# Performance work log

Hardware: AMD Instinct MI355X
Metric: run time of the kernel (lower is better)

## Reference

```python
import jax, jax.numpy as jnp
import numpy as np

NUM_EXPERTS = 8


def _ffn(x, w1, b1, w2, b2):
    # x: [T, H]; w1: [8H, H]; w2: [H, 4H]
    gu = x @ w1.T + b1                      # [T, 8H]
    gate, up = jnp.split(gu, 2, axis=-1)    # each [T, 4H]
    h = jax.nn.gelu(gate, approximate=True) * up
    return h @ w2.T + b2                    # [T, H]


def setup_inputs() -> dict:
    key = jax.random.key(0)
    ks = jax.random.split(key, 4)
    H, E, F = 1024, NUM_EXPERTS, 4096
    scale = 0.02
    return {
        "x": jax.random.normal(ks[0], (4, 1024, H), dtype=jnp.float32),
        "gate_w": jax.random.normal(ks[1], (E, H), dtype=jnp.float32) * scale,
        "gate_b": jnp.zeros((E,), dtype=jnp.float32),
        "w1": jax.random.normal(ks[2], (E, 2 * F, H), dtype=jnp.float32) * scale,
        "b1": jnp.zeros((E, 2 * F), dtype=jnp.float32),
        "w2": jax.random.normal(ks[3], (E, H, F), dtype=jnp.float32) * scale,
        "b2": jnp.zeros((E, H), dtype=jnp.float32),
    }


def reference(x, gate_w, gate_b, w1, b1, w2, b2):
    B, S, H = x.shape
    E = gate_w.shape[0]
    T = B * S
    xf = x.reshape(T, H)

    logits = xf @ gate_w.T + gate_b          # [T, E]
    probs = jax.nn.softmax(logits, axis=-1)
    vals, idx = jax.lax.top_k(probs, 2)      # [T, 2]

    # load balancing loss (matches torch bincount of top-1 expert)
    top1_onehot = jax.nn.one_hot(idx[:, 0], E, dtype=jnp.float32)
    frequencies = top1_onehot.sum(0) / T
    probability = probs.mean(0)
    load_balancing_loss = (probability * frequencies).mean() * float(E * E)

    # normalize top-2 scores
    total = vals.sum(axis=-1, keepdims=True)
    norm_scores = vals / total               # [T, 2]

    # per-token per-expert combine weights [T, E]
    weights = (jax.nn.one_hot(idx[:, 0], E, dtype=xf.dtype) * norm_scores[:, 0:1]
               + jax.nn.one_hot(idx[:, 1], E, dtype=xf.dtype) * norm_scores[:, 1:2])

    out = jnp.zeros_like(xf)
    for e in range(E):  # fixed small loop over experts
        out = out + weights[:, e:e + 1] * _ffn(xf, w1[e], b1[e], w2[e], b2[e])

    return out.reshape(B, S, H), load_balancing_loss
```

## Files before the change

kernel.cpp:

```cpp
#include <hip/hip_runtime.h>

#define T_TOK 4096
#define HDIM 1024
#define FDIM 4096
#define NEXP 8
#define ROWCAP 9216
#define NTILES_MAX 72

typedef __attribute__((ext_vector_type(8))) short short8;
typedef __attribute__((ext_vector_type(4))) float f32x4;

__device__ __forceinline__ unsigned short f2bf(float f) {
    unsigned int u = __builtin_bit_cast(unsigned int, f);
    u += 0x7fffu + ((u >> 16) & 1u);
    return (unsigned short)(u >> 16);
}

__device__ __forceinline__ float gelu_tanh(float x) {
    float z = 1.5957691216057308f * (x + 0.044715f * x * x * x);
    return x / (1.0f + __expf(-z));
}

__device__ __forceinline__ void gload16(const unsigned short* g, unsigned short* l) {
    __builtin_amdgcn_global_load_lds(
        (const __attribute__((address_space(1))) unsigned int*)g,
        (__attribute__((address_space(3))) unsigned int*)l, 16, 0, 0);
}

__global__ __launch_bounds__(256) void routing_kernel(
    const float* __restrict__ x, const float* __restrict__ gate_w,
    const float* __restrict__ gate_b,
    int* __restrict__ tokTop1, int* __restrict__ tokE,
    float* __restrict__ tokW, float* __restrict__ tokProbs)
{
    __shared__ float gws[NEXP * HDIM];
    int tid = threadIdx.x;
    for (int i = tid; i < NEXP * HDIM / 4; i += 256)
        ((float4*)gws)[i] = ((const float4*)gate_w)[i];
    __syncthreads();
    int lane = tid & 63;
    int t = blockIdx.x * 4 + (tid >> 6);
    float acc[NEXP];
    #pragma unroll
    for (int e = 0; e < NEXP; e++) acc[e] = 0.f;
    const float* xr = x + (size_t)t * HDIM;
    for (int k = lane; k < HDIM; k += 64) {
        float xv = xr[k];
        #pragma unroll
        for (int e = 0; e < NEXP; e++) acc[e] += xv * gws[e * HDIM + k];
    }
    #pragma unroll
    for (int e = 0; e < NEXP; e++) {
        #pragma unroll
        for (int off = 32; off >= 1; off >>= 1)
            acc[e] += __shfl_xor(acc[e], off);
    }
    if (lane == 0) {
        float m = -1e30f;
        #pragma unroll
        for (int e = 0; e < NEXP; e++) { acc[e] += gate_b[e]; m = fmaxf(m, acc[e]); }
        float p[NEXP]; float s = 0.f;
        #pragma unroll
        for (int e = 0; e < NEXP; e++) { p[e] = __expf(acc[e] - m); s += p[e]; }
        float inv = 1.f / s;
        int i0 = -1; float v0 = -1.f;
        #pragma unroll
        for (int e = 0; e < NEXP; e++) {
            p[e] *= inv;
            tokProbs[t * NEXP + e] = p[e];
            if (p[e] > v0) { v0 = p[e]; i0 = e; }
        }
        int i1 = -1; float v1 = -1.f;
        #pragma unroll
        for (int e = 0; e < NEXP; e++)
            if (e != i0 && p[e] > v1) { v1 = p[e]; i1 = e; }
        float tot = v0 + v1;
        tokTop1[t] = i0;
        tokE[2 * t] = i0; tokE[2 * t + 1] = i1;
        tokW[2 * t] = v0 / tot; tokW[2 * t + 1] = v1 / tot;
    }
}

__global__ __launch_bounds__(256) void stats_kernel(
    const int* __restrict__ tokTop1, const int* __restrict__ tokE,
    const float* __restrict__ tokProbs,
    int* __restrict__ counts, int* __restrict__ cnt1, float* __restrict__ probSum)
{
    int e = blockIdx.x, tid = threadIdx.x;
    float ps = 0.f; int c1 = 0, c = 0;
    for (int t = tid; t < T_TOK; t += 256) {
        ps += tokProbs[t * NEXP + e];
        c1 += (tokTop1[t] == e);
        c  += (tokE[2 * t] == e) + (tokE[2 * t + 1] == e);
    }
    __shared__ float sps[256]; __shared__ int sc1[256]; __shared__ int sc[256];
    sps[tid] = ps; sc1[tid] = c1; sc[tid] = c; __syncthreads();
    for (int s = 128; s > 0; s >>= 1) {
        if (tid < s) { sps[tid] += sps[tid + s]; sc1[tid] += sc1[tid + s]; sc[tid] += sc[tid + s]; }
        __syncthreads();
    }
    if (tid == 0) { probSum[e] = sps[0]; cnt1[e] = sc1[0]; counts[e] = sc[0]; }
}

__global__ void scan_loss_kernel(
    const int* __restrict__ counts, const int* __restrict__ cnt1,
    const float* __restrict__ probSum,
    int* __restrict__ offsets, int* __restrict__ cursor,
    int* __restrict__ tileE, int* __restrict__ nTiles,
    float* __restrict__ loss_out)
{
    int off = 0, nt = 0; float loss = 0.f;
    for (int e = 0; e < NEXP; e++) {
        offsets[e] = off;
        int pt = (counts[e] + 127) >> 7;
        for (int i = 0; i < pt; i++) tileE[nt++] = e;
        off += pt * 128;
        cursor[e] = 0;
        loss += probSum[e] * (float)cnt1[e];
    }
    nTiles[0] = nt;
    nTiles[1] = off;
    *loss_out = loss * 8.0f / ((float)T_TOK * (float)T_TOK);
}

__global__ __launch_bounds__(256) void assign_kernel(
    const int* __restrict__ tokE, const float* __restrict__ tokW,
    const int* __restrict__ offsets, int* __restrict__ cursor,
    int* __restrict__ rowTok, float* __restrict__ rowW)
{
    int t = blockIdx.x * 256 + threadIdx.x;
    #pragma unroll
    for (int s = 0; s < 2; s++) {
        int e = tokE[2 * t + s];
        int pos = atomicAdd(&cursor[e], 1);
        int row = offsets[e] + pos;
        rowTok[row] = t;
        rowW[row] = tokW[2 * t + s];
    }
}

__global__ __launch_bounds__(256) void convertw_kernel(
    const float* __restrict__ src, unsigned short* __restrict__ dst, long n8)
{
    long stride = (long)gridDim.x * 256;
    for (long i = (long)blockIdx.x * 256 + threadIdx.x; i < n8; i += stride) {
        const float4* s = (const float4*)src + 2 * i;
        float4 f0 = s[0], f1 = s[1];
        uint4 pk;
        pk.x = (unsigned)f2bf(f0.x) | ((unsigned)f2bf(f0.y) << 16);
        pk.y = (unsigned)f2bf(f0.z) | ((unsigned)f2bf(f0.w) << 16);
        pk.z = (unsigned)f2bf(f1.x) | ((unsigned)f2bf(f1.y) << 16);
        pk.w = (unsigned)f2bf(f1.z) | ((unsigned)f2bf(f1.w) << 16);
        ((uint4*)dst)[i] = pk;
    }
}

__global__ __launch_bounds__(256) void gather_kernel(
    const float* __restrict__ x, const int* __restrict__ rowTok,
    const int* __restrict__ offsets, const int* __restrict__ counts,
    const int* __restrict__ tileE, const int* __restrict__ nTiles,
    int chunkBase, unsigned short* __restrict__ Xc)
{
    int gr = chunkBase + blockIdx.x;
    if (gr >= nTiles[1]) return;
    int tid = threadIdx.x;
    int e = tileE[gr >> 7];
    ushort4* dst = (ushort4*)(Xc + (size_t)(gr - chunkBase) * HDIM);
    if (gr - offsets[e] < counts[e]) {
        int t = rowTok[gr];
        float4 v = ((const float4*)(x + (size_t)t * HDIM))[tid];
        ushort4 b;
        b.x = f2bf(v.x); b.y = f2bf(v.y); b.z = f2bf(v.z); b.w = f2bf(v.w);
        dst[tid] = b;
    } else {
        ushort4 z; z.x = 0; z.y = 0; z.z = 0; z.w = 0;
        dst[tid] = z;
    }
}

__global__ __launch_bounds__(256) void bias_out_kernel(
    const float* __restrict__ b2, const int* __restrict__ tokE,
    const float* __restrict__ tokW, float* __restrict__ out)
{
    int t = blockIdx.x, tid = threadIdx.x;
    int e0 = tokE[2 * t], e1 = tokE[2 * t + 1];
    float w0 = tokW[2 * t], w1 = tokW[2 * t + 1];
    float4 a = ((const float4*)(b2 + (size_t)e0 * HDIM))[tid];
    float4 b = ((const float4*)(b2 + (size_t)e1 * HDIM))[tid];
    float4 r;
    r.x = w0 * a.x + w1 * b.x; r.y = w0 * a.y + w1 * b.y;
    r.z = w0 * a.z + w1 * b.z; r.w = w0 * a.w + w1 * b.w;
    ((float4*)(out + (size_t)t * HDIM))[tid] = r;
}

template<bool WB>
__global__ __launch_bounds__(256) void gemm1_kernel(
    const unsigned short* __restrict__ Xc, const void* __restrict__ w1,
    const float* __restrict__ b1, const int* __restrict__ tileE,
    const int* __restrict__ nTiles, int chunkBase,
    unsigned short* __restrict__ hc)
{
    int gt = (chunkBase >> 7) + blockIdx.y;
    if (gt >= nTiles[0]) return;
    int e = tileE[gt];
    int localBase = gt * 128 - chunkBase;
    int cTile = blockIdx.x;

    __shared__ unsigned short As[128 * 64];
    __shared__ unsigned short Bs[128 * 64];

    int tid = threadIdx.x;
    int lane = tid & 63, wave = tid >> 6;
    int wm = wave & 1, wn = wave >> 1;
    int q = lane >> 4, c15 = lane & 15;

    const unsigned short* w1e_h = nullptr;
    const float* w1e_f = nullptr;
    if constexpr (WB) w1e_h = (const unsigned short*)w1 + (size_t)e * (2 * FDIM) * HDIM;
    else              w1e_f = (const float*)w1 + (size_t)e * (2 * FDIM) * HDIM;

    f32x4 accG[4][2], accU[4][2];
    #pragma unroll
    for (int a = 0; a < 4; a++)
        #pragma unroll
        for (int b = 0; b < 2; b++)
            #pragma unroll
            for (int c = 0; c < 4; c++) { accG[a][b][c] = 0.f; accU[a][b][c] = 0.f; }

    for (int k0 = 0; k0 < HDIM; k0 += 64) {
        __syncthreads();
        if constexpr (WB) {
            #pragma unroll
            for (int ci = 0; ci < 4; ci++) {
                int G = ci * 256 + wave * 64 + lane;
                int row = G >> 3;
                int gs = (lane & 7) ^ (row & 7);
                gload16(Xc + (size_t)(localBase + row) * HDIM + k0 + gs * 8,
                        As + (ci * 256 + wave * 64) * 8);
            }
            #pragma unroll
            for (int ci = 0; ci < 4; ci++) {
                int G = ci * 256 + wave * 64 + lane;
                int j = G >> 3;
                int gs = (lane & 7) ^ (j & 7);
                int w1row = (j < 64) ? (cTile * 64 + j) : (FDIM + cTile * 64 + (j - 64));
                gload16(w1e_h + (size_t)w1row * HDIM + k0 + gs * 8,
                        Bs + (ci * 256 + wave * 64) * 8);
            }
        } else {
            #pragma unroll
            for (int ci = 0; ci < 4; ci++) {
                int chunk = tid + 256 * ci;
                int i = chunk >> 3, kc = chunk & 7;
                uint4 av = *(const uint4*)(Xc + (size_t)(localBase + i) * HDIM + k0 + kc * 8);
                *(uint4*)(As + i * 64 + ((kc ^ (i & 7)) * 8)) = av;
            }
            #pragma unroll
            for (int ci = 0; ci < 4; ci++) {
                int chunk = tid + 256 * ci;
                int j = chunk >> 3, kc = chunk & 7;
                int w1row = (j < 64) ? (cTile * 64 + j) : (FDIM + cTile * 64 + (j - 64));
                const float* src = w1e_f + (size_t)w1row * HDIM + k0 + kc * 8;
                float4 f0 = *(const float4*)src;
                float4 f1 = *(const float4*)(src + 4);
                uint4 pk;
                pk.x = (unsigned)f2bf(f0.x) | ((unsigned)f2bf(f0.y) << 16);
                pk.y = (unsigned)f2bf(f0.z) | ((unsigned)f2bf(f0.w) << 16);
                pk.z = (unsigned)f2bf(f1.x) | ((unsigned)f2bf(f1.y) << 16);
                pk.w = (unsigned)f2bf(f1.z) | ((unsigned)f2bf(f1.w) << 16);
                *(uint4*)(Bs + j * 64 + ((kc ^ (j & 7)) * 8)) = pk;
            }
        }
        __syncthreads();
        #pragma unroll
        for (int kk = 0; kk < 64; kk += 32) {
            int slot = (((q + (kk >> 3)) ^ (c15 & 7)) & 7) * 8;
            short8 aF[4], bG[2], bU[2];
            #pragma unroll
            for (int mi = 0; mi < 4; mi++)
                aF[mi] = *(const short8*)(As + (wm * 64 + mi * 16 + c15) * 64 + slot);
            #pragma unroll
            for (int ni = 0; ni < 2; ni++) {
                bG[ni] = *(const short8*)(Bs + (wn * 32 + ni * 16 + c15) * 64 + slot);
                bU[ni] = *(const short8*)(Bs + (64 + wn * 32 + ni * 16 + c15) * 64 + slot);
            }
            #pragma unroll
            for (int mi = 0; mi < 4; mi++)
                #pragma unroll
                for (int ni = 0; ni < 2; ni++) {
                    accG[mi][ni] = __builtin_amdgcn_mfma_f32_16x16x32_bf16(aF[mi], bG[ni], accG[mi][ni], 0, 0, 0);
                    accU[mi][ni] = __builtin_amdgcn_mfma_f32_16x16x32_bf16(aF[mi], bU[ni], accU[mi][ni], 0, 0, 0);
                }
        }
    }
    const float* b1e = b1 + (size_t)e * (2 * FDIM);
    #pragma unroll
    for (int mi = 0; mi < 4; mi++)
        #pragma unroll
        for (int ni = 0; ni < 2; ni++) {
            int hcol = cTile * 64 + wn * 32 + ni * 16 + c15;
            float bg = b1e[hcol], bu = b1e[FDIM + hcol];
            #pragma unroll
            for (int r = 0; r < 4; r++) {
                int row = wm * 64 + mi * 16 + q * 4 + r;
                float g = accG[mi][ni][r] + bg;
                float u = accU[mi][ni][r] + bu;
                hc[(size_t)(localBase + row) * FDIM + hcol] = f2bf(gelu_tanh(g) * u);
            }
        }
}

template<bool WB>
__global__ __launch_bounds__(256) void gemm2_kernel(
    const unsigned short* __restrict__ hc, const void* __restrict__ w2,
    const int* __restrict__ offsets, const int* __restrict__ counts,
    const int* __restrict__ rowTok, const float* __restrict__ rowW,
    const int* __restrict__ tileE, const int* __restrict__ nTiles,
    int chunkBase, float* __restrict__ out)
{
    int gt = (chunkBase >> 7) + blockIdx.y;
    if (gt >= nTiles[0]) return;
    int e = tileE[gt];
    int localBase = gt * 128 - chunkBase;
    int rowBaseG = gt * 128;
    int cTile = blockIdx.x;

    __shared__ unsigned short As[128 * 64];
    __shared__ unsigned short Bs[128 * 64];

    int tid = threadIdx.x;
    int lane = tid & 63, wave = tid >> 6;
    int wm = wave & 1, wn = wave >> 1;
    int q = lane >> 4, c15 = lane & 15;

    const unsigned short* w2e_h = nullptr;
    const float* w2e_f = nullptr;
    if constexpr (WB) w2e_h = (const unsigned short*)w2 + (size_t)e * HDIM * FDIM;
    else              w2e_f = (const float*)w2 + (size_t)e * HDIM * FDIM;

    f32x4 acc[4][4];
    #pragma unroll
    for (int a = 0; a < 4; a++)
        #pragma unroll
        for (int b = 0; b < 4; b++)
            #pragma unroll
            for (int c = 0; c < 4; c++) acc[a][b][c] = 0.f;

    for (int k0 = 0; k0 < FDIM; k0 += 64) {
        __syncthreads();
        if constexpr (WB) {
            #pragma unroll
            for (int ci = 0; ci < 4; ci++) {
                int G = ci * 256 + wave * 64 + lane;
                int row = G >> 3;
                int gs = (lane & 7) ^ (row & 7);
                gload16(hc + (size_t)(localBase + row) * FDIM + k0 + gs * 8,
                        As + (ci * 256 + wave * 64) * 8);
            }
            #pragma unroll
            for (int ci = 0; ci < 4; ci++) {
                int G = ci * 256 + wave * 64 + lane;
                int j = G >> 3;
                int gs = (lane & 7) ^ (j & 7);
                gload16(w2e_h + (size_t)(cTile * 128 + j) * FDIM + k0 + gs * 8,
                        Bs + (ci * 256 + wave * 64) * 8);
            }
        } else {
            #pragma unroll
            for (int ci = 0; ci < 4; ci++) {
                int chunk = tid + 256 * ci;
                int i = chunk >> 3, kc = chunk & 7;
                uint4 av = *(const uint4*)(hc + (size_t)(localBase + i) * FDIM + k0 + kc * 8);
                *(uint4*)(As + i * 64 + ((kc ^ (i & 7)) * 8)) = av;
            }
            #pragma unroll
            for (int ci = 0; ci < 4; ci++) {
                int chunk = tid + 256 * ci;
                int j = chunk >> 3, kc = chunk & 7;
                const float* src = w2e_f + (size_t)(cTile * 128 + j) * FDIM + k0 + kc * 8;
                float4 f0 = *(const float4*)src;
                float4 f1 = *(const float4*)(src + 4);
                uint4 pk;
                pk.x = (unsigned)f2bf(f0.x) | ((unsigned)f2bf(f0.y) << 16);
                pk.y = (unsigned)f2bf(f0.z) | ((unsigned)f2bf(f0.w) << 16);
                pk.z = (unsigned)f2bf(f1.x) | ((unsigned)f2bf(f1.y) << 16);
                pk.w = (unsigned)f2bf(f1.z) | ((unsigned)f2bf(f1.w) << 16);
                *(uint4*)(Bs + j * 64 + ((kc ^ (j & 7)) * 8)) = pk;
            }
        }
        __syncthreads();
        #pragma unroll
        for (int kk = 0; kk < 64; kk += 32) {
            int slot = (((q + (kk >> 3)) ^ (c15 & 7)) & 7) * 8;
            short8 aF[4], bF[4];
            #pragma unroll
            for (int mi = 0; mi < 4; mi++)
                aF[mi] = *(const short8*)(As + (wm * 64 + mi * 16 + c15) * 64 + slot);
            #pragma unroll
            for (int ni = 0; ni < 4; ni++)
                bF[ni] = *(const short8*)(Bs + (wn * 64 + ni * 16 + c15) * 64 + slot);
            #pragma unroll
            for (int mi = 0; mi < 4; mi++)
                #pragma unroll
                for (int ni = 0; ni < 4; ni++)
                    acc[mi][ni] = __builtin_amdgcn_mfma_f32_16x16x32_bf16(aF[mi], bF[ni], acc[mi][ni], 0, 0, 0);
        }
    }
    #pragma unroll
    for (int mi = 0; mi < 4; mi++) {
        #pragma unroll
        for (int r = 0; r < 4; r++) {
            int row = wm * 64 + mi * 16 + q * 4 + r;
            int grow = rowBaseG + row;
            if (grow - offsets[e] < counts[e]) {
                int t = rowTok[grow];
                float w = rowW[grow];
                float* od = out + (size_t)t * HDIM + cTile * 128 + wn * 64 + c15;
                #pragma unroll
                for (int ni = 0; ni < 4; ni++)
                    atomicAdd(od + ni * 16, w * acc[mi][ni][r]);
            }
        }
    }
}

extern "C" void kernel_launch(void* const* d_in, const int* in_sizes, int n_in,
                              void* d_out, int out_size, void* d_ws, size_t ws_size,
                              hipStream_t stream) {
    (void)in_sizes; (void)n_in; (void)out_size;
    const float* x      = (const float*)d_in[0];
    const float* gate_w = (const float*)d_in[1];
    const float* gate_b = (const float*)d_in[2];
    const float* w1     = (const float*)d_in[3];
    const float* b1     = (const float*)d_in[4];
    const float* w2     = (const float*)d_in[5];
    const float* b2     = (const float*)d_in[6];
    float* out = (float*)d_out;

    char* ws = (char*)d_ws;
    int*   counts   = (int*)(ws + 0);
    int*   cnt1     = (int*)(ws + 32);
    int*   cursor   = (int*)(ws + 64);
    int*   offsets  = (int*)(ws + 96);
    float* probSum  = (float*)(ws + 128);
    int*   nTiles   = (int*)(ws + 160);
    int*   tileE    = (int*)(ws + 256);
    int*   tokTop1  = (int*)(ws + 1024);
    int*   tokE     = (int*)(ws + 1024 + 16384);
    float* tokW     = (float*)(ws + 1024 + 49152);
    float* tokProbs = (float*)(ws + 1024 + 81920);
    int*   rowTok   = (int*)(ws + 1024 + 212992);
    float* rowW     = (float*)(ws + 1024 + 249856);
    const size_t fixedEnd = 512 * 1024;

    const size_t W1E = (size_t)NEXP * 2 * FDIM * HDIM;
    const size_t W2E = (size_t)NEXP * HDIM * FDIM;
    const size_t WBYTES = (W1E + W2E) * 2;
    bool wbf16 = ws_size >= fixedEnd + WBYTES + (size_t)128 * (HDIM + FDIM) * 2;

    unsigned short* w1b = nullptr;
    unsigned short* w2b = nullptr;
    size_t chunkStart = fixedEnd;
    if (wbf16) {
        w1b = (unsigned short*)(ws + fixedEnd);
        w2b = w1b + W1E;
        chunkStart = fixedEnd + WBYTES;
    }

    size_t avail = ws_size > chunkStart ? ws_size - chunkStart : 0;
    int ch = (int)((avail / (10240ULL * 128ULL)) * 128ULL);
    if (ch > ROWCAP) ch = ROWCAP;
    if (ch < 128) ch = 128;
    unsigned short* Xc = (unsigned short*)(ws + chunkStart);
    unsigned short* hc = (unsigned short*)(ws + chunkStart + (size_t)ch * HDIM * 2);
    int nChunks = (ROWCAP + ch - 1) / ch;

    if (wbf16) {
        convertw_kernel<<<2048, 256, 0, stream>>>(w1, w1b, (long)(W1E / 8));
        convertw_kernel<<<2048, 256, 0, stream>>>(w2, w2b, (long)(W2E / 8));
    }

    routing_kernel<<<T_TOK / 4, 256, 0, stream>>>(x, gate_w, gate_b, tokTop1, tokE, tokW, tokProbs);
    stats_kernel<<<NEXP, 256, 0, stream>>>(tokTop1, tokE, tokProbs, counts, cnt1, probSum);
    scan_loss_kernel<<<1, 1, 0, stream>>>(counts, cnt1, probSum, offsets, cursor, tileE, nTiles,
                                          out + (size_t)T_TOK * HDIM);
    assign_kernel<<<T_TOK / 256, 256, 0, stream>>>(tokE, tokW, offsets, cursor, rowTok, rowW);
    bias_out_kernel<<<T_TOK, 256, 0, stream>>>(b2, tokE, tokW, out);

    for (int c = 0; c < nChunks; c++) {
        int base = c * ch;
        int rows = ROWCAP - base; if (rows > ch) rows = ch;
        int tiles = rows >> 7;
        gather_kernel<<<rows, 256, 0, stream>>>(x, rowTok, offsets, counts, tileE, nTiles, base, Xc);
        if (wbf16) {
            gemm1_kernel<true><<<dim3(FDIM / 64, tiles), 256, 0, stream>>>(
                Xc, (const void*)w1b, b1, tileE, nTiles, base, hc);
            gemm2_kernel<true><<<dim3(HDIM / 128, tiles), 256, 0, stream>>>(
                hc, (const void*)w2b, offsets, counts, rowTok, rowW, tileE, nTiles, base, out);
        } else {
            gemm1_kernel<false><<<dim3(FDIM / 64, tiles), 256, 0, stream>>>(
                Xc, (const void*)w1, b1, tileE, nTiles, base, hc);
            gemm2_kernel<false><<<dim3(HDIM / 128, tiles), 256, 0, stream>>>(
                hc, (const void*)w2, offsets, counts, rowTok, rowW, tileE, nTiles, base, out);
        }
    }
}
```

Baseline: 986.2 us.

## Stage GEMM2 output in buffer and scatter with separate atomic kernel

GEMM2 now computes the transposed product (weights as A, activations as B), so each lane holds four consecutive output columns and can write float4 rows into a new fp32 staging buffer. It no longer does per-element scattered atomicAdds into the output. A new scatter kernel reads each staged row and atomically adds the weighted values into the token's output row. This trades scattered, strided atomics in the GEMM epilogue for coalesced stores plus an extra pass over the staging buffer. The workspace requirement per row grows, which may reduce chunk size or disable the bf16 weight cache.

```diff
diff --git a/kernel.cpp b/kernel.cpp
--- a/kernel.cpp
+++ b/kernel.cpp
@@ -193,6 +193,28 @@
     ((float4*)(out + (size_t)t * HDIM))[tid] = r;
 }
 
+__global__ __launch_bounds__(256) void scatter_kernel(
+    const float* __restrict__ ybuf, const int* __restrict__ rowTok,
+    const float* __restrict__ rowW,
+    const int* __restrict__ offsets, const int* __restrict__ counts,
+    const int* __restrict__ tileE, const int* __restrict__ nTiles,
+    int chunkBase, float* __restrict__ out)
+{
+    int gr = chunkBase + blockIdx.x;
+    if (gr >= nTiles[1]) return;
+    int e = tileE[gr >> 7];
+    if (gr - offsets[e] >= counts[e]) return;
+    int t = rowTok[gr];
+    float w = rowW[gr];
+    int tid = threadIdx.x;
+    float4 y = ((const float4*)(ybuf + (size_t)(gr - chunkBase) * HDIM))[tid];
+    float* od = out + (size_t)t * HDIM + tid * 4;
+    atomicAdd(od + 0, w * y.x);
+    atomicAdd(od + 1, w * y.y);
+    atomicAdd(od + 2, w * y.z);
+    atomicAdd(od + 3, w * y.w);
+}
+
 template<bool WB>
 __global__ __launch_bounds__(256) void gemm1_kernel(
     const unsigned short* __restrict__ Xc, const void* __restrict__ w1,
@@ -313,16 +335,13 @@
 template<bool WB>
 __global__ __launch_bounds__(256) void gemm2_kernel(
     const unsigned short* __restrict__ hc, const void* __restrict__ w2,
-    const int* __restrict__ offsets, const int* __restrict__ counts,
-    const int* __restrict__ rowTok, const float* __restrict__ rowW,
     const int* __restrict__ tileE, const int* __restrict__ nTiles,
-    int chunkBase, float* __restrict__ out)
+    int chunkBase, float* __restrict__ ybuf)
 {
     int gt = (chunkBase >> 7) + blockIdx.y;
     if (gt >= nTiles[0]) return;
     int e = tileE[gt];
     int localBase = gt * 128 - chunkBase;
-    int rowBaseG = gt * 128;
     int cTile = blockIdx.x;
 
     __shared__ unsigned short As[128 * 64];
@@ -392,34 +411,30 @@
         #pragma unroll
         for (int kk = 0; kk < 64; kk += 32) {
             int slot = (((q + (kk >> 3)) ^ (c15 & 7)) & 7) * 8;
-            short8 aF[4], bF[4];
+            short8 aW[4], bT[4];
             #pragma unroll
             for (int mi = 0; mi < 4; mi++)
-                aF[mi] = *(const short8*)(As + (wm * 64 + mi * 16 + c15) * 64 + slot);
+                aW[mi] = *(const short8*)(Bs + (wm * 64 + mi * 16 + c15) * 64 + slot);
             #pragma unroll
             for (int ni = 0; ni < 4; ni++)
-                bF[ni] = *(const short8*)(Bs + (wn * 64 + ni * 16 + c15) * 64 + slot);
+                bT[ni] = *(const short8*)(As + (wn * 64 + ni * 16 + c15) * 64 + slot);
             #pragma unroll
             for (int mi = 0; mi < 4; mi++)
                 #pragma unroll
                 for (int ni = 0; ni < 4; ni++)
-                    acc[mi][ni] = __builtin_amdgcn_mfma_f32_16x16x32_bf16(aF[mi], bF[ni], acc[mi][ni], 0, 0, 0);
-        }
-    }
-    #pragma unroll
-    for (int mi = 0; mi < 4; mi++) {
-        #pragma unroll
-        for (int r = 0; r < 4; r++) {
-            int row = wm * 64 + mi * 16 + q * 4 + r;
-            int grow = rowBaseG + row;
-            if (grow - offsets[e] < counts[e]) {
-                int t = rowTok[grow];
-                float w = rowW[grow];
-                float* od = out + (size_t)t * HDIM + cTile * 128 + wn * 64 + c15;
-                #pragma unroll
-                for (int ni = 0; ni < 4; ni++)
-                    atomicAdd(od + ni * 16, w * acc[mi][ni][r]);
-            }
+                    acc[mi][ni] = __builtin_amdgcn_mfma_f32_16x16x32_bf16(aW[mi], bT[ni], acc[mi][ni], 0, 0, 0);
+        }
+    }
+    #pragma unroll
+    for (int ni = 0; ni < 4; ni++) {
+        int lrow = localBase + wn * 64 + ni * 16 + c15;
+        float* yd = ybuf + (size_t)lrow * HDIM + cTile * 128 + wm * 64 + q * 4;
+        #pragma unroll
+        for (int mi = 0; mi < 4; mi++) {
+            float4 v;
+            v.x = acc[mi][ni][0]; v.y = acc[mi][ni][1];
+            v.z = acc[mi][ni][2]; v.w = acc[mi][ni][3];
+            *(float4*)(yd + mi * 16) = v;
         }
     }
 }
@@ -456,7 +471,7 @@
     const size_t W1E = (size_t)NEXP * 2 * FDIM * HDIM;
     const size_t W2E = (size_t)NEXP * HDIM * FDIM;
     const size_t WBYTES = (W1E + W2E) * 2;
-    bool wbf16 = ws_size >= fixedEnd + WBYTES + (size_t)128 * (HDIM + FDIM) * 2;
+    bool wbf16 = ws_size >= fixedEnd + WBYTES + (size_t)128 * 14336;
 
     unsigned short* w1b = nullptr;
     unsigned short* w2b = nullptr;
@@ -468,11 +483,12 @@
     }
 
     size_t avail = ws_size > chunkStart ? ws_size - chunkStart : 0;
-    int ch = (int)((avail / (10240ULL * 128ULL)) * 128ULL);
+    int ch = (int)((avail / (14336ULL * 128ULL)) * 128ULL);
     if (ch > ROWCAP) ch = ROWCAP;
     if (ch < 128) ch = 128;
     unsigned short* Xc = (unsigned short*)(ws + chunkStart);
     unsigned short* hc = (unsigned short*)(ws + chunkStart + (size_t)ch * HDIM * 2);
+    float* ybuf = (float*)(ws + chunkStart + (size_t)ch * HDIM * 2 + (size_t)ch * FDIM * 2);
     int nChunks = (ROWCAP + ch - 1) / ch;
 
     if (wbf16) {
@@ -496,12 +512,14 @@
             gemm1_kernel<true><<<dim3(FDIM / 64, tiles), 256, 0, stream>>>(
                 Xc, (const void*)w1b, b1, tileE, nTiles, base, hc);
             gemm2_kernel<true><<<dim3(HDIM / 128, tiles), 256, 0, stream>>>(
-                hc, (const void*)w2b, offsets, counts, rowTok, rowW, tileE, nTiles, base, out);
+                hc, (const void*)w2b, tileE, nTiles, base, ybuf);
         } else {
             gemm1_kernel<false><<<dim3(FDIM / 64, tiles), 256, 0, stream>>>(
                 Xc, (const void*)w1, b1, tileE, nTiles, base, hc);
             gemm2_kernel<false><<<dim3(HDIM / 128, tiles), 256, 0, stream>>>(
-                hc, (const void*)w2, offsets, counts, rowTok, rowW, tileE, nTiles, base, out);
-        }
-    }
-}
+                hc, (const void*)w2, tileE, nTiles, base, ybuf);
+        }
+        scatter_kernel<<<rows, 256, 0, stream>>>(ybuf, rowTok, rowW, offsets, counts,
+                                                 tileE, nTiles, base, out);
+    }
+}
```

New measurement: 1.014 ms. +2.8%, slower.
